# Optimization experiments

Measured on AMD Instinct MI355X. Metric: run time of the kernel, lower is better.

The kernel has to match this reference:

```python
import jax, jax.numpy as jnp
import numpy as np
import math

NUM_HEADS = 16
NUM_KV_HEADS = 4
HEAD_DIM = 128


def rotate_half(x):
    x1, x2 = x[..., : x.shape[-1] // 2], x[..., x.shape[-1] // 2 :]
    return jnp.concatenate((-x2, x1), axis=-1)


def setup_inputs() -> dict:
    key = jax.random.key(0)
    ks = jax.random.split(key, 7)
    B, L, D = 2, 2048, 2048
    hidden_states = jax.random.normal(ks[0], (B, L, D), dtype=jnp.float32)
    # realistic RoPE tables
    inv_freq = 1.0 / (10000.0 ** (np.arange(0, HEAD_DIM, 2, dtype=np.float32) / HEAD_DIM))
    t = np.arange(L, dtype=np.float32)
    freqs = np.outer(t, inv_freq)
    emb = np.concatenate([freqs, freqs], axis=-1)
    cos = jnp.asarray(np.cos(emb), dtype=jnp.float32)
    sin = jnp.asarray(np.sin(emb), dtype=jnp.float32)
    s = 1.0 / math.sqrt(D)
    Wq = jax.random.normal(ks[1], (D, NUM_HEADS * HEAD_DIM), dtype=jnp.float32) * s
    Wk = jax.random.normal(ks[2], (D, NUM_KV_HEADS * HEAD_DIM), dtype=jnp.float32) * s
    Wv = jax.random.normal(ks[3], (D, NUM_KV_HEADS * HEAD_DIM), dtype=jnp.float32) * s
    Wo = jax.random.normal(ks[4], (NUM_HEADS * HEAD_DIM, D), dtype=jnp.float32) * s
    return {"hidden_states": hidden_states, "cos": cos, "sin": sin,
            "Wq": Wq, "Wk": Wk, "Wv": Wv, "Wo": Wo}


def reference(hidden_states, cos, sin, Wq, Wk, Wv, Wo):
    B, L, D = hidden_states.shape
    H, KVH, Dh = NUM_HEADS, NUM_KV_HEADS, HEAD_DIM
    q = (hidden_states @ Wq).reshape(B, L, H, Dh)
    k = (hidden_states @ Wk).reshape(B, L, KVH, Dh)
    v = (hidden_states @ Wv).reshape(B, L, KVH, Dh)
    # RoPE: cos/sin are [L, Dh] broadcast over batch and heads
    c = cos[None, :, None, :]
    s = sin[None, :, None, :]
    q = q * c + rotate_half(q) * s
    k = k * c + rotate_half(k) * s
    # GQA: repeat kv heads to match query heads
    rep = H // KVH
    k = jnp.repeat(k, rep, axis=2)
    v = jnp.repeat(v, rep, axis=2)
    scale = 1.0 / math.sqrt(Dh)
    # [B, H, L, L]
    attn = jnp.einsum('bqhd,bkhd->bhqk', q, k) * scale
    i = jnp.arange(L)[:, None]
    j = jnp.arange(L)[None, :]
    attn = jnp.where(i >= j, attn, -jnp.inf)
    attn = jax.nn.softmax(attn, axis=-1)
    out = jnp.einsum('bhqk,bkhd->bqhd', attn, v).reshape(B, L, H * Dh)
    return out @ Wo
```

## Files before the change

kernel.cpp:

```cpp
#include <hip/hip_runtime.h>
#include <hip/hip_bf16.h>

typedef __attribute__((ext_vector_type(8))) short bf16x8;
typedef __attribute__((ext_vector_type(4))) float f32x4;
typedef __attribute__((ext_vector_type(4))) short short4v;

__device__ __forceinline__ unsigned short f2bf(float f) {
  union { float f; unsigned u; } x; x.f = f;
  return (unsigned short)((x.u + 0x7FFFu + ((x.u >> 16) & 1u)) >> 16);
}

__device__ __forceinline__ short f2bf_hw(float f) {
  __hip_bfloat16 h = __float2bfloat16(f);
  return *(short*)&h;
}

__device__ __forceinline__ void lds_cp16(const void* g, void* l) {
  __builtin_amdgcn_global_load_lds(
      (const __attribute__((address_space(1))) void*)g,
      (__attribute__((address_space(3))) void*)l,
      16, 0, 0);
}

#define GBAR() do { __builtin_amdgcn_s_barrier(); __builtin_amdgcn_sched_barrier(0); } while (0)

__global__ __launch_bounds__(256) void cast_x(const float* __restrict__ in,
                                              short* __restrict__ out, int n4) {
  int i = blockIdx.x * 256 + threadIdx.x;
  if (i >= n4) return;
  float4 v = reinterpret_cast<const float4*>(in)[i];
  short4v o;
  o.x = (short)f2bf(v.x); o.y = (short)f2bf(v.y);
  o.z = (short)f2bf(v.z); o.w = (short)f2bf(v.w);
  reinterpret_cast<short4v*>(out)[i] = o;
}

__global__ __launch_bounds__(256) void transp_w(const float* __restrict__ Wq,
                                                const float* __restrict__ Wk,
                                                const float* __restrict__ Wv,
                                                const float* __restrict__ Wo,
                                                short* __restrict__ Wqkv,
                                                short* __restrict__ Wot) {
  __shared__ float t[32][33];
  const int K = 2048;
  int bnG = blockIdx.x * 32;
  int bk = blockIdx.y * 32;
  const float* src; int N, bn; short* out; int orow;
  if (bnG < 2048)      { src = Wq; N = 2048; bn = bnG;        out = Wqkv; orow = bnG; }
  else if (bnG < 2560) { src = Wk; N = 512;  bn = bnG - 2048; out = Wqkv; orow = bnG; }
  else if (bnG < 3072) { src = Wv; N = 512;  bn = bnG - 2560; out = Wqkv; orow = bnG; }
  else                 { src = Wo; N = 2048; bn = bnG - 3072; out = Wot;  orow = bnG - 3072; }
  int tx = threadIdx.x, ty = threadIdx.y;
  for (int i = ty; i < 32; i += 8)
    t[i][tx] = src[(size_t)(bk + i) * N + bn + tx];
  __syncthreads();
  for (int i = ty; i < 32; i += 8)
    out[(size_t)(orow + i) * K + bk + tx] = (short)f2bf(t[tx][i]);
}

__global__ __launch_bounds__(256) void transp_v(const short* __restrict__ V,
                                                short* __restrict__ VTo) {
  __shared__ short t[32][34];
  const int hd = blockIdx.z;
  const int p0 = blockIdx.x * 32, d0 = blockIdx.y * 32;
  const short* src = V + (size_t)hd * 2048 * 128;
  short* dst = VTo + (size_t)hd * 2048 * 128;
  int tx = threadIdx.x, ty = threadIdx.y;
  for (int i = ty; i < 32; i += 8)
    t[i][tx] = src[(size_t)(p0 + i) * 128 + d0 + tx];
  __syncthreads();
  for (int i = ty; i < 32; i += 8)
    dst[(size_t)(d0 + i) * 2048 + p0 + tx] = t[tx][i];
}

__global__ __launch_bounds__(512, 2) void gemm_qkv(
    const short* __restrict__ A, const short* __restrict__ Bt,
    short* __restrict__ Qo, short* __restrict__ Ko, short* __restrict__ Vo,
    const float* __restrict__ cosT, const float* __restrict__ sinT) {
  constexpr int NM = 4;
  __shared__ __align__(16) short As[2][256 * 64];
  __shared__ __align__(16) short Bs[2][256 * 64];
  const int tid = threadIdx.x;
  const int l = tid & 63, l15 = l & 15, l4 = l >> 4;
  const int wid = tid >> 6, wr = wid >> 1, wc = wid & 1;
  const int sid = (blockIdx.x & 7) * 24 + (blockIdx.x >> 3);
  const int bm = sid % 16, bn = sid / 16;

  const int srow = tid >> 3;
  const int sch = tid & 7;

  auto stA = [&](int dbuf, int k0, int i) {
    const int rl = srow + i * 64;
    const int c = sch ^ (rl & 7);
    lds_cp16(A + (size_t)(bm * 256 + rl) * 2048 + k0 + c * 8,
             (char*)As[dbuf] + tid * 16 + i * 8192);
  };
  auto stB = [&](int dbuf, int k0, int j) {
    const int rl = srow + j * 64;
    const int c = sch ^ (rl & 7);
    lds_cp16(Bt + (size_t)(bn * 256 + rl) * 2048 + k0 + c * 8,
             (char*)Bs[dbuf] + tid * 16 + j * 8192);
  };
  auto rdA = [&](int dbuf, int m, int kb) {
    const int row = wr * 64 + m * 16 + l15;
    return *(const bf16x8*)((const char*)As[dbuf] + (row << 7) +
                            ((kb * 64 + l4 * 16) ^ ((row & 7) << 4)));
  };
  auto rdB = [&](int dbuf, int nh, int f, int kb) {
    const int row = wc * 128 + nh * 64 + f * 16 + l15;
    return *(const bf16x8*)((const char*)Bs[dbuf] + (row << 7) +
                            ((kb * 64 + l4 * 16) ^ ((row & 7) << 4)));
  };

  f32x4 acc[NM][8];
#pragma unroll
  for (int m = 0; m < NM; m++)
#pragma unroll
    for (int n = 0; n < 8; n++) acc[m][n] = (f32x4){0.f, 0.f, 0.f, 0.f};

  const int NT = 32;

#pragma unroll
  for (int i = 0; i < NM; i++) stA(0, 0, i);
#pragma unroll
  for (int j = 0; j < 4; j++) stB(0, 0, j);
  asm volatile("s_waitcnt vmcnt(0)" ::: "memory");
  GBAR();

  for (int kt = 0; kt < NT; kt++) {
    const int buf = kt & 1, nbf = buf ^ 1;
    const bool stg = (kt + 1 < NT);
    const int k1 = (kt + 1) << 6;
    bf16x8 a[NM], b[4];

#pragma unroll
    for (int m = 0; m < NM; m++) a[m] = rdA(buf, m, 0);
#pragma unroll
    for (int f = 0; f < 4; f++) b[f] = rdB(buf, 0, f, 0);
    if (stg) { stA(nbf, k1, 0); stA(nbf, k1, 1); }
    if (stg) asm volatile("s_waitcnt vmcnt(2)" ::: "memory");
    else     asm volatile("s_waitcnt vmcnt(0)" ::: "memory");
    GBAR();
    asm volatile("s_waitcnt lgkmcnt(0)" ::: "memory");
    __builtin_amdgcn_sched_barrier(0);
    __builtin_amdgcn_s_setprio(1);
#pragma unroll
    for (int m = 0; m < NM; m++)
#pragma unroll
      for (int f = 0; f < 4; f++)
        acc[m][f] = __builtin_amdgcn_mfma_f32_16x16x32_bf16(a[m], b[f], acc[m][f], 0, 0, 0);
    __builtin_amdgcn_s_setprio(0);
    GBAR();

#pragma unroll
    for (int f = 0; f < 4; f++) b[f] = rdB(buf, 1, f, 0);
    if (stg) { stA(nbf, k1, 2); stA(nbf, k1, 3); }
    GBAR();
    asm volatile("s_waitcnt lgkmcnt(0)" ::: "memory");
    __builtin_amdgcn_sched_barrier(0);
    __builtin_amdgcn_s_setprio(1);
#pragma unroll
    for (int m = 0; m < NM; m++)
#pragma unroll
      for (int f = 0; f < 4; f++)
        acc[m][4 + f] = __builtin_amdgcn_mfma_f32_16x16x32_bf16(a[m], b[f], acc[m][4 + f], 0, 0, 0);
    __builtin_amdgcn_s_setprio(0);
    GBAR();

#pragma unroll
    for (int m = 0; m < NM; m++) a[m] = rdA(buf, m, 1);
#pragma unroll
    for (int f = 0; f < 4; f++) b[f] = rdB(buf, 0, f, 1);
    if (stg) { stB(nbf, k1, 0); stB(nbf, k1, 2); }
    GBAR();
    asm volatile("s_waitcnt lgkmcnt(0)" ::: "memory");
    __builtin_amdgcn_sched_barrier(0);
    __builtin_amdgcn_s_setprio(1);
#pragma unroll
    for (int m = 0; m < NM; m++)
#pragma unroll
      for (int f = 0; f < 4; f++)
        acc[m][f] = __builtin_amdgcn_mfma_f32_16x16x32_bf16(a[m], b[f], acc[m][f], 0, 0, 0);
    __builtin_amdgcn_s_setprio(0);
    GBAR();

#pragma unroll
    for (int f = 0; f < 4; f++) b[f] = rdB(buf, 1, f, 1);
    if (stg) { stB(nbf, k1, 1); stB(nbf, k1, 3); }
    if (stg) asm volatile("s_waitcnt vmcnt(2)" ::: "memory");
    GBAR();
    asm volatile("s_waitcnt lgkmcnt(0)" ::: "memory");
    __builtin_amdgcn_sched_barrier(0);
    __builtin_amdgcn_s_setprio(1);
#pragma unroll
    for (int m = 0; m < NM; m++)
#pragma unroll
      for (int f = 0; f < 4; f++)
        acc[m][4 + f] = __builtin_amdgcn_mfma_f32_16x16x32_bf16(a[m], b[f], acc[m][4 + f], 0, 0, 0);
    __builtin_amdgcn_s_setprio(0);
    GBAR();
  }

  {
    const int head = bn * 2 + wc;
#pragma unroll
    for (int m = 0; m < NM; m++) {
#pragma unroll
      for (int r = 0; r < 4; r++) {
        const int grow = bm * 256 + wr * 64 + m * 16 + l4 * 4 + r;
        const int bb = grow >> 11, pos = grow & 2047;
        if (head < 20) {
          float c4[4], s4[4];
#pragma unroll
          for (int ni = 0; ni < 4; ni++) {
            const int dh = ni * 16 + l15;
            c4[ni] = cosT[pos * 128 + dh];
            s4[ni] = sinT[pos * 128 + dh];
          }
          short* dst;
          if (head < 16) dst = Qo + ((size_t)(bb * 16 + head) * 2048 + pos) * 128;
          else           dst = Ko + ((size_t)(bb * 4 + (head - 16)) * 2048 + pos) * 128;
#pragma unroll
          for (int ni = 0; ni < 4; ni++) {
            const int dh = ni * 16 + l15;
            float xlo = acc[m][ni][r], xhi = acc[m][ni + 4][r];
            dst[dh]      = (short)f2bf(xlo * c4[ni] - xhi * s4[ni]);
            dst[dh + 64] = (short)f2bf(xhi * c4[ni] + xlo * s4[ni]);
          }
        } else {
          short* dst = Vo + ((size_t)(bb * 4 + (head - 20)) * 2048 + pos) * 128;
#pragma unroll
          for (int ni = 0; ni < 8; ni++)
            dst[(ni >> 2) * 64 + (ni & 3) * 16 + l15] = (short)f2bf(acc[m][ni][r]);
        }
      }
    }
  }
}

__global__ __launch_bounds__(512, 2) void gemm_op(
    const short* __restrict__ A, const short* __restrict__ Bt,
    float* __restrict__ C) {
  __shared__ __align__(16) short As[2][128 * 64];
  __shared__ __align__(16) short Bs[2][128 * 64];
  const int tid = threadIdx.x;
  const int l = tid & 63, l15 = l & 15, l4 = l >> 4;
  const int wid = tid >> 6, wr = wid >> 1, wc = wid & 1;
  const int sid = (blockIdx.x & 7) * 64 + (blockIdx.x >> 3);
  const int bm = sid & 31, bn = sid >> 5;
  const int srow = tid >> 3;
  const int sch = tid & 7;

  auto stA = [&](int dbuf, int k0, int i) {
    const int rl = i * 64 + srow;
    const int c = sch ^ (rl & 7);
    lds_cp16(A + (size_t)(bm * 128 + rl) * 2048 + k0 + c * 8,
             (char*)As[dbuf] + i * 8192 + tid * 16);
  };
  auto stB = [&](int dbuf, int k0, int j) {
    const int rl = j * 64 + srow;
    const int c = sch ^ (rl & 7);
    lds_cp16(Bt + (size_t)(bn * 128 + rl) * 2048 + k0 + c * 8,
             (char*)Bs[dbuf] + j * 8192 + tid * 16);
  };
  auto rdA = [&](int dbuf, int m, int kb) {
    const int row = wr * 32 + m * 16 + l15;
    return *(const bf16x8*)((const char*)As[dbuf] + (row << 7) +
                            ((kb * 64 + l4 * 16) ^ ((row & 7) << 4)));
  };
  auto rdB = [&](int dbuf, int nh, int f, int kb) {
    const int row = nh * 64 + wc * 32 + f * 16 + l15;
    return *(const bf16x8*)((const char*)Bs[dbuf] + (row << 7) +
                            ((kb * 64 + l4 * 16) ^ ((row & 7) << 4)));
  };

  f32x4 acc[2][4];
#pragma unroll
  for (int m = 0; m < 2; m++)
#pragma unroll
    for (int n = 0; n < 4; n++) acc[m][n] = (f32x4){0.f, 0.f, 0.f, 0.f};

  const int NT = 32;

  stB(0, 0, 0); stA(0, 0, 0); stA(0, 0, 1); stB(0, 0, 1);
  asm volatile("s_waitcnt vmcnt(1)" ::: "memory");
  GBAR();

  for (int kt = 0; kt < NT; kt++) {
    const int buf = kt & 1, nbf = buf ^ 1;
    const bool stg = (kt + 1 < NT);
    const int k1 = (kt + 1) << 6;
    bf16x8 a[2][2], b[2];

#pragma unroll
    for (int m = 0; m < 2; m++) a[m][0] = rdA(buf, m, 0);
#pragma unroll
    for (int f = 0; f < 2; f++) b[f] = rdB(buf, 0, f, 0);
    if (stg) stB(nbf, k1, 0);
    GBAR();
    asm volatile("s_waitcnt lgkmcnt(0)" ::: "memory");
    __builtin_amdgcn_sched_barrier(0);
    __builtin_amdgcn_s_setprio(1);
#pragma unroll
    for (int m = 0; m < 2; m++)
#pragma unroll
      for (int f = 0; f < 2; f++)
        acc[m][f] = __builtin_amdgcn_mfma_f32_16x16x32_bf16(a[m][0], b[f], acc[m][f], 0, 0, 0);
    __builtin_amdgcn_s_setprio(0);
    GBAR();

#pragma unroll
    for (int m = 0; m < 2; m++) a[m][1] = rdA(buf, m, 1);
#pragma unroll
    for (int f = 0; f < 2; f++) b[f] = rdB(buf, 0, f, 1);
    if (stg) stA(nbf, k1, 0);
    if (stg) asm volatile("s_waitcnt vmcnt(2)" ::: "memory");
    else     asm volatile("s_waitcnt vmcnt(0)" ::: "memory");
    GBAR();
    asm volatile("s_waitcnt lgkmcnt(0)" ::: "memory");
    __builtin_amdgcn_sched_barrier(0);
    __builtin_amdgcn_s_setprio(1);
#pragma unroll
    for (int m = 0; m < 2; m++)
#pragma unroll
      for (int f = 0; f < 2; f++)
        acc[m][f] = __builtin_amdgcn_mfma_f32_16x16x32_bf16(a[m][1], b[f], acc[m][f], 0, 0, 0);
    __builtin_amdgcn_s_setprio(0);
    GBAR();

#pragma unroll
    for (int f = 0; f < 2; f++) b[f] = rdB(buf, 1, f, 0);
    if (stg) stA(nbf, k1, 1);
    GBAR();
    asm volatile("s_waitcnt lgkmcnt(0)" ::: "memory");
    __builtin_amdgcn_sched_barrier(0);
    __builtin_amdgcn_s_setprio(1);
#pragma unroll
    for (int m = 0; m < 2; m++)
#pragma unroll
      for (int f = 0; f < 2; f++)
        acc[m][2 + f] = __builtin_amdgcn_mfma_f32_16x16x32_bf16(a[m][0], b[f], acc[m][2 + f], 0, 0, 0);
    __builtin_amdgcn_s_setprio(0);
    GBAR();

#pragma unroll
    for (int f = 0; f < 2; f++) b[f] = rdB(buf, 1, f, 1);
    if (stg) stB(nbf, k1, 1);
    if (stg) asm volatile("s_waitcnt vmcnt(1)" ::: "memory");
    else     asm volatile("s_waitcnt vmcnt(0)" ::: "memory");
    GBAR();
    asm volatile("s_waitcnt lgkmcnt(0)" ::: "memory");
    __builtin_amdgcn_sched_barrier(0);
    __builtin_amdgcn_s_setprio(1);
#pragma unroll
    for (int m = 0; m < 2; m++)
#pragma unroll
      for (int f = 0; f < 2; f++)
        acc[m][2 + f] = __builtin_amdgcn_mfma_f32_16x16x32_bf16(a[m][1], b[f], acc[m][2 + f], 0, 0, 0);
    __builtin_amdgcn_s_setprio(0);
    GBAR();
  }

#pragma unroll
  for (int m = 0; m < 2; m++) {
    const int grow = bm * 128 + wr * 32 + m * 16 + l4 * 4;
#pragma unroll
    for (int n = 0; n < 4; n++) {
      const int col = bn * 128 + (n >> 1) * 64 + wc * 32 + (n & 1) * 16 + l15;
#pragma unroll
      for (int r = 0; r < 4; r++)
        C[(size_t)(grow + r) * 2048 + col] = acc[m][n][r];
    }
  }
}

__global__ __launch_bounds__(256) void attn_fwd(
    const short* __restrict__ Q, const short* __restrict__ K,
    const short* __restrict__ VT, short* __restrict__ AO) {
  __shared__ __align__(16) short Ks[2][64 * 128];
  __shared__ __align__(16) short VTs[2][128 * 64];
  __shared__ __align__(16) short Pl[4][16 * 64];
  const int tid = threadIdx.x;
  const int w = tid >> 6, l = tid & 63;
  const int l15 = l & 15, l4 = l >> 4;
  const int bid = blockIdx.x;
  const int lg = (bid & 7) * 64 + (bid >> 3);
  const int bh = lg >> 4, pp = lg & 15;
  const int b = bh >> 4, h = bh & 15, kv = h >> 2;
  const short* Qbase = Q + (size_t)(b * 16 + h) * 2048 * 128;
  const short* Kbase = K + (size_t)(b * 4 + kv) * 2048 * 128;
  const short* VTb   = VT + (size_t)(b * 4 + kv) * 2048 * 128;

  int rk[4], ck[4], dv[4], kc[4];
#pragma unroll
  for (int i = 0; i < 4; i++) {
    const int c = tid + i * 256;
    rk[i] = c >> 4; ck[i] = (c & 15) ^ (rk[i] & 7);
    dv[i] = c >> 3; kc[i] = (c & 7) ^ (dv[i] & 7);
  }

  const float SCL = 0.08838834764831845f * 1.4426950408889634f;

  bf16x8 ones;
#pragma unroll
  for (int j = 0; j < 8; j++) ones[j] = (short)0x3F80;

  for (int qq = 0; qq < 2; qq++) {
    const int qt = qq ? (31 - pp) : pp;
    const int q0w = qt * 64 + w * 16;

    bf16x8 qf[4];
#pragma unroll
    for (int kb = 0; kb < 4; kb++)
      qf[kb] = *(const bf16x8*)(Qbase + (size_t)(q0w + l15) * 128 + kb * 32 + l4 * 8);

    f32x4 oacc[8];
#pragma unroll
    for (int i = 0; i < 8; i++) oacc[i] = (f32x4){0.f, 0.f, 0.f, 0.f};
    f32x4 lacc = (f32x4){0.f, 0.f, 0.f, 0.f};

    const int ntiles = qt + 1;

    __syncthreads();
#pragma unroll
    for (int i = 0; i < 4; i++) {
      lds_cp16(Kbase + rk[i] * 128 + ck[i] * 8, (char*)Ks[0] + i * 4096 + tid * 16);
      lds_cp16(VTb + (size_t)dv[i] * 2048 + kc[i] * 8, (char*)VTs[0] + i * 4096 + tid * 16);
    }

    for (int nt = 0; nt < ntiles; nt++) {
      const int k0 = nt * 64, buf = nt & 1;
      __syncthreads();
      if (nt + 1 < ntiles) {
        const int kn = k0 + 64, bnx = buf ^ 1;
#pragma unroll
        for (int i = 0; i < 4; i++) {
          lds_cp16(Kbase + (size_t)(kn + rk[i]) * 128 + ck[i] * 8,
                   (char*)Ks[bnx] + i * 4096 + tid * 16);
          lds_cp16(VTb + (size_t)dv[i] * 2048 + kn + kc[i] * 8,
                   (char*)VTs[bnx] + i * 4096 + tid * 16);
        }
      }

      f32x4 sa[4];
#pragma unroll
      for (int kg = 0; kg < 4; kg++) sa[kg] = (f32x4){0.f, 0.f, 0.f, 0.f};
      __builtin_amdgcn_s_setprio(1);
#pragma unroll
      for (int kg = 0; kg < 4; kg++) {
        const int row = kg * 16 + l15;
        const int swz = (row & 7) << 4;
#pragma unroll
        for (int kb = 0; kb < 4; kb++) {
          const char* kp = (const char*)Ks[buf] + row * 256 + ((kb * 64 + l4 * 16) ^ swz);
          sa[kg] = __builtin_amdgcn_mfma_f32_16x16x32_bf16(qf[kb], *(const bf16x8*)kp, sa[kg], 0, 0, 0);
        }
      }
      __builtin_amdgcn_s_setprio(0);

      float p[4][4];
      const bool domask = (k0 + 63 > q0w);
#pragma unroll
      for (int kg = 0; kg < 4; kg++)
#pragma unroll
        for (int r = 0; r < 4; r++) {
          float pv = exp2f(sa[kg][r] * SCL);
          if (domask) {
            int qrow = q0w + l4 * 4 + r;
            if (k0 + kg * 16 + l15 > qrow) pv = 0.f;
          }
          p[kg][r] = pv;
        }

#pragma unroll
      for (int r = 0; r < 4; r++) {
        const int rw = l4 * 4 + r;
        const int swz = (rw & 7) << 4;
#pragma unroll
        for (int kg = 0; kg < 4; kg++)
          *(short*)((char*)Pl[w] + (rw * 128 + ((kg * 32 + l15 * 2) ^ swz))) =
              f2bf_hw(p[kg][r]);
      }
      asm volatile("s_waitcnt lgkmcnt(0)" ::: "memory");
      bf16x8 pf[2];
#pragma unroll
      for (int ks = 0; ks < 2; ks++)
        pf[ks] = *(const bf16x8*)((const char*)Pl[w] +
                 (l15 * 128 + ((ks * 64 + l4 * 16) ^ ((l15 & 7) << 4))));

      __builtin_amdgcn_s_setprio(1);
#pragma unroll
      for (int nb = 0; nb < 8; nb++) {
        const int d = nb * 16 + l15;
        const int dsw = (d & 7) << 4;
#pragma unroll
        for (int ks = 0; ks < 2; ks++) {
          const char* vp = (const char*)VTs[buf] + d * 128 + ((ks * 64 + l4 * 16) ^ dsw);
          oacc[nb] = __builtin_amdgcn_mfma_f32_16x16x32_bf16(pf[ks], *(const bf16x8*)vp, oacc[nb], 0, 0, 0);
        }
      }
      lacc = __builtin_amdgcn_mfma_f32_16x16x32_bf16(pf[0], ones, lacc, 0, 0, 0);
      lacc = __builtin_amdgcn_mfma_f32_16x16x32_bf16(pf[1], ones, lacc, 0, 0, 0);
      __builtin_amdgcn_s_setprio(0);
    }

#pragma unroll
    for (int r = 0; r < 4; r++) {
      float inv = 1.0f / lacc[r];
      size_t rowb = ((size_t)b * 2048 + q0w + l4 * 4 + r) * 2048 + h * 128;
#pragma unroll
      for (int nb = 0; nb < 8; nb++)
        AO[rowb + nb * 16 + l15] = f2bf_hw(oacc[nb][r] * inv);
    }
  }
}

extern "C" void kernel_launch(void* const* d_in, const int* in_sizes, int n_in,
                              void* d_out, int out_size, void* d_ws, size_t ws_size,
                              hipStream_t stream) {
  const float* hs   = (const float*)d_in[0];
  const float* cosT = (const float*)d_in[1];
  const float* sinT = (const float*)d_in[2];
  const float* Wq   = (const float*)d_in[3];
  const float* Wk   = (const float*)d_in[4];
  const float* Wv   = (const float*)d_in[5];
  const float* Wo   = (const float*)d_in[6];
  float* out = (float*)d_out;

  char* p = (char*)d_ws;
  short* Xb   = (short*)p; p += (size_t)4096 * 2048 * 2;
  short* Wqkv = (short*)p; p += (size_t)3072 * 2048 * 2;
  short* Wot  = (short*)p; p += (size_t)2048 * 2048 * 2;
  short* Qb   = (short*)p; p += (size_t)2 * 16 * 2048 * 128 * 2;
  short* Kb   = (short*)p; p += (size_t)2 * 4 * 2048 * 128 * 2;
  short* Vb   = (short*)p; p += (size_t)2 * 4 * 2048 * 128 * 2;
  short* VTb  = (short*)p; p += (size_t)2 * 4 * 2048 * 128 * 2;
  short* AO   = Xb;

  cast_x<<<8192, 256, 0, stream>>>(hs, Xb, 2097152);
  transp_w<<<dim3(160, 64), dim3(32, 8), 0, stream>>>(Wq, Wk, Wv, Wo, Wqkv, Wot);

  gemm_qkv<<<192, 512, 0, stream>>>(Xb, Wqkv, Qb, Kb, Vb, cosT, sinT);
  transp_v<<<dim3(64, 4, 8), dim3(32, 8), 0, stream>>>(Vb, VTb);
  attn_fwd<<<512, 256, 0, stream>>>(Qb, Kb, VTb, AO);
  gemm_op<<<512, 512, 0, stream>>>(AO, Wot, out);
}
```

Before: 202.8 us.

## Retile QKV GEMM to 256x192 tiles with permuted weight columns for RoPE

New measurement: 203.3 us. No clear change (+0.2%).

```diff
diff --git a/kernel.cpp b/kernel.cpp
--- a/kernel.cpp
+++ b/kernel.cpp
@@ -45,17 +45,23 @@
   const int K = 2048;
   int bnG = blockIdx.x * 32;
   int bk = blockIdx.y * 32;
-  const float* src; int N, bn; short* out; int orow;
-  if (bnG < 2048)      { src = Wq; N = 2048; bn = bnG;        out = Wqkv; orow = bnG; }
-  else if (bnG < 2560) { src = Wk; N = 512;  bn = bnG - 2048; out = Wqkv; orow = bnG; }
-  else if (bnG < 3072) { src = Wv; N = 512;  bn = bnG - 2560; out = Wqkv; orow = bnG; }
-  else                 { src = Wo; N = 2048; bn = bnG - 3072; out = Wot;  orow = bnG - 3072; }
+  const float* src; int N, bn; short* out; int orow; bool perm;
+  if (bnG < 2048)      { src = Wq; N = 2048; bn = bnG;        out = Wqkv; orow = bnG;        perm = true; }
+  else if (bnG < 2560) { src = Wk; N = 512;  bn = bnG - 2048; out = Wqkv; orow = bnG;        perm = true; }
+  else if (bnG < 3072) { src = Wv; N = 512;  bn = bnG - 2560; out = Wqkv; orow = bnG;        perm = true; }
+  else                 { src = Wo; N = 2048; bn = bnG - 3072; out = Wot;  orow = bnG - 3072; perm = false; }
   int tx = threadIdx.x, ty = threadIdx.y;
   for (int i = ty; i < 32; i += 8)
     t[i][tx] = src[(size_t)(bk + i) * N + bn + tx];
   __syncthreads();
-  for (int i = ty; i < 32; i += 8)
-    out[(size_t)(orow + i) * K + bk + tx] = (short)f2bf(t[tx][i]);
+  for (int i = ty; i < 32; i += 8) {
+    int c = orow + i;
+    if (perm) {
+      const int d = c & 127, hi = d >> 6, d6 = d & 63;
+      c = (c & ~127) | (((d6 >> 4) << 5) | (hi << 4) | (d6 & 15));
+    }
+    out[(size_t)c * K + bk + tx] = (short)f2bf(t[tx][i]);
+  }
 }
 
 __global__ __launch_bounds__(256) void transp_v(const short* __restrict__ V,
@@ -73,18 +79,17 @@
     dst[(size_t)(d0 + i) * 2048 + p0 + tx] = t[tx][i];
 }
 
-__global__ __launch_bounds__(512, 2) void gemm_qkv(
+__global__ __launch_bounds__(512, 1) void gemm_qkv(
     const short* __restrict__ A, const short* __restrict__ Bt,
     short* __restrict__ Qo, short* __restrict__ Ko, short* __restrict__ Vo,
     const float* __restrict__ cosT, const float* __restrict__ sinT) {
-  constexpr int NM = 4;
   __shared__ __align__(16) short As[2][256 * 64];
-  __shared__ __align__(16) short Bs[2][256 * 64];
+  __shared__ __align__(16) short Bs[2][192 * 64];
   const int tid = threadIdx.x;
   const int l = tid & 63, l15 = l & 15, l4 = l >> 4;
   const int wid = tid >> 6, wr = wid >> 1, wc = wid & 1;
-  const int sid = (blockIdx.x & 7) * 24 + (blockIdx.x >> 3);
-  const int bm = sid % 16, bn = sid / 16;
+  const int sid = (blockIdx.x & 7) * 32 + (blockIdx.x >> 3);
+  const int bm = sid & 15, bn = sid >> 4;
 
   const int srow = tid >> 3;
   const int sch = tid & 7;
@@ -95,11 +100,13 @@
     lds_cp16(A + (size_t)(bm * 256 + rl) * 2048 + k0 + c * 8,
              (char*)As[dbuf] + tid * 16 + i * 8192);
   };
-  auto stB = [&](int dbuf, int k0, int j) {
-    const int rl = srow + j * 64;
-    const int c = sch ^ (rl & 7);
-    lds_cp16(Bt + (size_t)(bn * 256 + rl) * 2048 + k0 + c * 8,
-             (char*)Bs[dbuf] + tid * 16 + j * 8192);
+  auto stB = [&](int dbuf, int k0, int q) {
+    if (tid < 384) {
+      const int rl = q * 48 + (tid >> 3);
+      const int c = sch ^ (rl & 7);
+      lds_cp16(Bt + (size_t)(bn * 192 + rl) * 2048 + k0 + c * 8,
+               (char*)Bs[dbuf] + q * 6144 + tid * 16);
+    }
   };
   auto rdA = [&](int dbuf, int m, int kb) {
     const int row = wr * 64 + m * 16 + l15;
@@ -107,23 +114,23 @@
                             ((kb * 64 + l4 * 16) ^ ((row & 7) << 4)));
   };
   auto rdB = [&](int dbuf, int nh, int f, int kb) {
-    const int row = wc * 128 + nh * 64 + f * 16 + l15;
+    const int row = wc * 96 + nh * 48 + f * 16 + l15;
     return *(const bf16x8*)((const char*)Bs[dbuf] + (row << 7) +
                             ((kb * 64 + l4 * 16) ^ ((row & 7) << 4)));
   };
 
-  f32x4 acc[NM][8];
-#pragma unroll
-  for (int m = 0; m < NM; m++)
-#pragma unroll
-    for (int n = 0; n < 8; n++) acc[m][n] = (f32x4){0.f, 0.f, 0.f, 0.f};
+  f32x4 acc[4][6];
+#pragma unroll
+  for (int m = 0; m < 4; m++)
+#pragma unroll
+    for (int n = 0; n < 6; n++) acc[m][n] = (f32x4){0.f, 0.f, 0.f, 0.f};
 
   const int NT = 32;
 
 #pragma unroll
-  for (int i = 0; i < NM; i++) stA(0, 0, i);
-#pragma unroll
-  for (int j = 0; j < 4; j++) stB(0, 0, j);
+  for (int i = 0; i < 4; i++) stA(0, 0, i);
+#pragma unroll
+  for (int q = 0; q < 4; q++) stB(0, 0, q);
   asm volatile("s_waitcnt vmcnt(0)" ::: "memory");
   GBAR();
 
@@ -131,12 +138,12 @@
     const int buf = kt & 1, nbf = buf ^ 1;
     const bool stg = (kt + 1 < NT);
     const int k1 = (kt + 1) << 6;
-    bf16x8 a[NM], b[4];
-
-#pragma unroll
-    for (int m = 0; m < NM; m++) a[m] = rdA(buf, m, 0);
-#pragma unroll
-    for (int f = 0; f < 4; f++) b[f] = rdB(buf, 0, f, 0);
+    bf16x8 a[4], b[3];
+
+#pragma unroll
+    for (int m = 0; m < 4; m++) a[m] = rdA(buf, m, 0);
+#pragma unroll
+    for (int f = 0; f < 3; f++) b[f] = rdB(buf, 0, f, 0);
     if (stg) { stA(nbf, k1, 0); stA(nbf, k1, 1); }
     if (stg) asm volatile("s_waitcnt vmcnt(2)" ::: "memory");
     else     asm volatile("s_waitcnt vmcnt(0)" ::: "memory");
@@ -145,47 +152,47 @@
     __builtin_amdgcn_sched_barrier(0);
     __builtin_amdgcn_s_setprio(1);
 #pragma unroll
-    for (int m = 0; m < NM; m++)
-#pragma unroll
-      for (int f = 0; f < 4; f++)
+    for (int m = 0; m < 4; m++)
+#pragma unroll
+      for (int f = 0; f < 3; f++)
         acc[m][f] = __builtin_amdgcn_mfma_f32_16x16x32_bf16(a[m], b[f], acc[m][f], 0, 0, 0);
     __builtin_amdgcn_s_setprio(0);
     GBAR();
 
 #pragma unroll
-    for (int f = 0; f < 4; f++) b[f] = rdB(buf, 1, f, 0);
+    for (int f = 0; f < 3; f++) b[f] = rdB(buf, 1, f, 0);
     if (stg) { stA(nbf, k1, 2); stA(nbf, k1, 3); }
     GBAR();
     asm volatile("s_waitcnt lgkmcnt(0)" ::: "memory");
     __builtin_amdgcn_sched_barrier(0);
     __builtin_amdgcn_s_setprio(1);
 #pragma unroll
-    for (int m = 0; m < NM; m++)
-#pragma unroll
-      for (int f = 0; f < 4; f++)
-        acc[m][4 + f] = __builtin_amdgcn_mfma_f32_16x16x32_bf16(a[m], b[f], acc[m][4 + f], 0, 0, 0);
-    __builtin_amdgcn_s_setprio(0);
-    GBAR();
-
-#pragma unroll
-    for (int m = 0; m < NM; m++) a[m] = rdA(buf, m, 1);
-#pragma unroll
-    for (int f = 0; f < 4; f++) b[f] = rdB(buf, 0, f, 1);
+    for (int m = 0; m < 4; m++)
+#pragma unroll
+      for (int f = 0; f < 3; f++)
+        acc[m][3 + f] = __builtin_amdgcn_mfma_f32_16x16x32_bf16(a[m], b[f], acc[m][3 + f], 0, 0, 0);
+    __builtin_amdgcn_s_setprio(0);
+    GBAR();
+
+#pragma unroll
+    for (int m = 0; m < 4; m++) a[m] = rdA(buf, m, 1);
+#pragma unroll
+    for (int f = 0; f < 3; f++) b[f] = rdB(buf, 0, f, 1);
     if (stg) { stB(nbf, k1, 0); stB(nbf, k1, 2); }
     GBAR();
     asm volatile("s_waitcnt lgkmcnt(0)" ::: "memory");
     __builtin_amdgcn_sched_barrier(0);
     __builtin_amdgcn_s_setprio(1);
 #pragma unroll
-    for (int m = 0; m < NM; m++)
-#pragma unroll
-      for (int f = 0; f < 4; f++)
+    for (int m = 0; m < 4; m++)
+#pragma unroll
+      for (int f = 0; f < 3; f++)
         acc[m][f] = __builtin_amdgcn_mfma_f32_16x16x32_bf16(a[m], b[f], acc[m][f], 0, 0, 0);
     __builtin_amdgcn_s_setprio(0);
     GBAR();
 
 #pragma unroll
-    for (int f = 0; f < 4; f++) b[f] = rdB(buf, 1, f, 1);
+    for (int f = 0; f < 3; f++) b[f] = rdB(buf, 1, f, 1);
     if (stg) { stB(nbf, k1, 1); stB(nbf, k1, 3); }
     if (stg) asm volatile("s_waitcnt vmcnt(2)" ::: "memory");
     GBAR();
@@ -193,45 +200,38 @@
     __builtin_amdgcn_sched_barrier(0);
     __builtin_amdgcn_s_setprio(1);
 #pragma unroll
-    for (int m = 0; m < NM; m++)
-#pragma unroll
-      for (int f = 0; f < 4; f++)
-        acc[m][4 + f] = __builtin_amdgcn_mfma_f32_16x16x32_bf16(a[m], b[f], acc[m][4 + f], 0, 0, 0);
-    __builtin_amdgcn_s_setprio(0);
-    GBAR();
-  }
-
-  {
-    const int head = bn * 2 + wc;
-#pragma unroll
-    for (int m = 0; m < NM; m++) {
-#pragma unroll
-      for (int r = 0; r < 4; r++) {
-        const int grow = bm * 256 + wr * 64 + m * 16 + l4 * 4 + r;
-        const int bb = grow >> 11, pos = grow & 2047;
+    for (int m = 0; m < 4; m++)
+#pragma unroll
+      for (int f = 0; f < 3; f++)
+        acc[m][3 + f] = __builtin_amdgcn_mfma_f32_16x16x32_bf16(a[m], b[f], acc[m][3 + f], 0, 0, 0);
+    __builtin_amdgcn_s_setprio(0);
+    GBAR();
+  }
+
+#pragma unroll
+  for (int m = 0; m < 4; m++) {
+#pragma unroll
+    for (int r = 0; r < 4; r++) {
+      const int grow = bm * 256 + wr * 64 + m * 16 + l4 * 4 + r;
+      const int bb = grow >> 11, pos = grow & 2047;
+#pragma unroll
+      for (int p = 0; p < 3; p++) {
+        const int x_lo = bn * 192 + wc * 96 + p * 32 + l15;
+        const int head = x_lo >> 7;
+        const int dh = ((x_lo >> 5) & 3) * 16 + l15;
+        const float xlo = acc[m][2 * p][r], xhi = acc[m][2 * p + 1][r];
         if (head < 20) {
-          float c4[4], s4[4];
-#pragma unroll
-          for (int ni = 0; ni < 4; ni++) {
-            const int dh = ni * 16 + l15;
-            c4[ni] = cosT[pos * 128 + dh];
-            s4[ni] = sinT[pos * 128 + dh];
-          }
+          const float cv = cosT[pos * 128 + dh];
+          const float sv = sinT[pos * 128 + dh];
           short* dst;
           if (head < 16) dst = Qo + ((size_t)(bb * 16 + head) * 2048 + pos) * 128;
           else           dst = Ko + ((size_t)(bb * 4 + (head - 16)) * 2048 + pos) * 128;
-#pragma unroll
-          for (int ni = 0; ni < 4; ni++) {
-            const int dh = ni * 16 + l15;
-            float xlo = acc[m][ni][r], xhi = acc[m][ni + 4][r];
-            dst[dh]      = (short)f2bf(xlo * c4[ni] - xhi * s4[ni]);
-            dst[dh + 64] = (short)f2bf(xhi * c4[ni] + xlo * s4[ni]);
-          }
+          dst[dh]      = (short)f2bf(xlo * cv - xhi * sv);
+          dst[dh + 64] = (short)f2bf(xhi * cv + xlo * sv);
         } else {
           short* dst = Vo + ((size_t)(bb * 4 + (head - 20)) * 2048 + pos) * 128;
-#pragma unroll
-          for (int ni = 0; ni < 8; ni++)
-            dst[(ni >> 2) * 64 + (ni & 3) * 16 + l15] = (short)f2bf(acc[m][ni][r]);
+          dst[dh]      = (short)f2bf(xlo);
+          dst[dh + 64] = (short)f2bf(xhi);
         }
       }
     }
@@ -540,7 +540,7 @@
   cast_x<<<8192, 256, 0, stream>>>(hs, Xb, 2097152);
   transp_w<<<dim3(160, 64), dim3(32, 8), 0, stream>>>(Wq, Wk, Wv, Wo, Wqkv, Wot);
 
-  gemm_qkv<<<192, 512, 0, stream>>>(Xb, Wqkv, Qb, Kb, Vb, cosT, sinT);
+  gemm_qkv<<<256, 512, 0, stream>>>(Xb, Wqkv, Qb, Kb, Vb, cosT, sinT);
   transp_v<<<dim3(64, 4, 8), dim3(32, 8), 0, stream>>>(Vb, VTb);
   attn_fwd<<<512, 256, 0, stream>>>(Qb, Kb, VTb, AO);
   gemm_op<<<512, 512, 0, stream>>>(AO, Wot, out);
```
